# Performance work log

Hardware: AMD Instinct MI355X
Metric: run time of the kernel (lower is better)

The kernel has to match this reference:

```python
import jax, jax.numpy as jnp
import numpy as np

F_MAX = 16  # static max number of frames (torch code uses max(frames) dynamically)
B, C, H, W = 8, 5, 512, 512


def setup_inputs() -> dict:
    key = jax.random.key(0)
    k1, k2 = jax.random.split(key)
    inp = jax.random.normal(k1, (B, C, H, W), dtype=jnp.float32)
    frames = jax.random.randint(k2, (B,), 1, F_MAX + 1)  # n_frames per sample in [1, F_MAX]
    return {"input": inp, "frames": frames}


def _acquire(inp, frames, noise_key):
    b, _, h, w = inp.shape
    ku, kn = jax.random.split(noise_key)
    img = inp[:, :1]                                                   # [B,1,H,W]
    bias = jax.nn.relu(jnp.mean(inp[:, 1:2], axis=(1, 2, 3), keepdims=True))  # [B,1,1,1]
    sampled = img + bias                                               # broadcasts to [B,F_MAX,H,W] below
    center = img + bias                                                # [B,1,H,W]
    # Frechet noise
    fw = jax.nn.relu(inp[:, 2:3])                                      # weight [B,1,H,W]
    fa = jax.nn.relu(inp[:, 3:4])                                      # alpha  [B,1,H,W]
    u = jnp.clip(jax.random.uniform(ku, (b, F_MAX, h, w), dtype=inp.dtype), 1e-6, 1.0 - 1e-6)
    sampled = sampled + fw * (-jnp.log(u)) ** (-fa)                    # [B,F_MAX,H,W]
    center = center + fw * (1.0 / (fa + 1.0)) ** fa
    # Gaussian noise
    gw = jax.nn.relu(inp[:, 4:5])
    sampled = sampled + gw * jax.random.normal(kn, (b, F_MAX, h, w), dtype=inp.dtype)
    acquired_frames = jnp.clip(sampled, 0.0, 1.0)                      # [B,F_MAX,H,W]
    # ragged per-sample mean over first n_frames frames, vectorized via mask
    mask = (jnp.arange(F_MAX)[None, :, None, None] < frames[:, None, None, None]).astype(inp.dtype)
    frames_f = frames.astype(inp.dtype)[:, None, None, None]
    acquired = jnp.sum(acquired_frames * mask, axis=1, keepdims=True) / frames_f  # [B,1,H,W]
    return acquired, jnp.clip(center, 0.0, 1.0)


def reference(input, frames):
    return _acquire(input, frames, jax.random.key(42))
```

## Files before the change

kernel.cpp:

```cpp
#include <hip/hip_runtime.h>
#include <stdint.h>

#define HW 262144
#define ACQ_N 2097152
#define SREG 69632
#define NREG3 208896

#define CNT(b, c) ((((b) << 2) | (c)) << 5)

#define LOG2F(x) __builtin_amdgcn_logf(x)
#define EXP2F(x) __builtin_amdgcn_exp2f(x)
#define SQRTF(x) __builtin_amdgcn_sqrtf(x)
#define RCPF(x)  __builtin_amdgcn_rcpf(x)

#define ROTL(x, r) __builtin_amdgcn_alignbit((x), (x), (32 - (r)) & 31)

static inline void tf2x32_host(uint32_t k0, uint32_t k1, uint32_t c0, uint32_t c1,
                               uint32_t& o0, uint32_t& o1) {
  const uint32_t ks2 = k0 ^ k1 ^ 0x1BD11BDAu;
  uint32_t x0 = c0 + k0, x1 = c1 + k1;
#define TFR(r) { x0 += x1; x1 = (x1 << (r)) | (x1 >> (32 - (r))); x1 ^= x0; }
  TFR(13) TFR(15) TFR(26) TFR(6)
  x0 += k1;  x1 += ks2 + 1u;
  TFR(17) TFR(29) TFR(16) TFR(24)
  x0 += ks2; x1 += k0 + 2u;
  TFR(13) TFR(15) TFR(26) TFR(6)
  x0 += k0;  x1 += k1 + 3u;
  TFR(17) TFR(29) TFR(16) TFR(24)
  x0 += k1;  x1 += ks2 + 4u;
  TFR(13) TFR(15) TFR(26) TFR(6)
  x0 += ks2; x1 += k0 + 5u;
#undef TFR
  o0 = x0; o1 = x1;
}

__device__ __forceinline__ uint32_t rbits32(uint32_t k0, uint32_t k1, uint32_t idx) {
  const uint32_t ks2 = k0 ^ k1 ^ 0x1BD11BDAu;
  uint32_t x0 = k0, x1 = idx + k1;
#define TFR(r) { x0 += x1; x1 = ROTL(x1, r); x1 ^= x0; }
  TFR(13) TFR(15) TFR(26) TFR(6)
  x0 += k1;  x1 += ks2 + 1u;
  TFR(17) TFR(29) TFR(16) TFR(24)
  x0 += ks2; x1 += k0 + 2u;
  TFR(13) TFR(15) TFR(26) TFR(6)
  x0 += k0;  x1 += k1 + 3u;
  TFR(17) TFR(29) TFR(16) TFR(24)
  x0 += k1;  x1 += ks2 + 4u;
  TFR(13) TFR(15) TFR(26) TFR(6)
  x0 += ks2; x1 += k0 + 5u;
#undef TFR
  return x0 ^ x1;
}

__device__ __forceinline__ float unit_from_bits(uint32_t b) {
  return __uint_as_float((b >> 9) | 0x3F800000u) - 1.0f;
}

__device__ __forceinline__ float sqrt2_erfinv(float x) {
  float ome = fmaf(-x, x, 1.0f);
  float w = -0.69314718056f * LOG2F(ome);
  float wn = w - 2.5f;
  float p = 3.974065e-08f;
  p = fmaf(p, wn, 4.854641e-07f);
  p = fmaf(p, wn, -4.982823e-06f);
  p = fmaf(p, wn, -6.210531e-06f);
  p = fmaf(p, wn, 3.091200e-04f);
  p = fmaf(p, wn, -1.773035e-03f);
  p = fmaf(p, wn, -5.908135e-03f);
  p = fmaf(p, wn, 3.488029e-01f);
  p = fmaf(p, wn, 2.123314e+00f);
  if (__builtin_expect(w >= 5.0f, 0)) {
    float wf = SQRTF(w) - 3.0f;
    float q = -2.831458e-04f;
    q = fmaf(q, wf, 1.427657e-04f);
    q = fmaf(q, wf, 1.908260e-03f);
    q = fmaf(q, wf, -5.195013e-03f);
    q = fmaf(q, wf, 8.116892e-03f);
    q = fmaf(q, wf, -1.0779791e-02f);
    q = fmaf(q, wf, 1.3348579e-02f);
    q = fmaf(q, wf, 1.416582e+00f);
    q = fmaf(q, wf, 4.006434e+00f);
    p = q;
  }
  return p * x;
}

__device__ __forceinline__ float loop_fg(float base, float fw, float fa, float gw,
                                         uint32_t idx, int nf,
                                         uint32_t ku0, uint32_t ku1,
                                         uint32_t kn0, uint32_t kn1) {
  float nfa = -fa, fac = fa * 0.52876637294f;
  float acc = 0.0f;
#pragma unroll 2
  for (int f = 0; f < nf; ++f) {
    uint32_t ub = rbits32(ku0, ku1, idx);
    uint32_t nb = rbits32(kn0, kn1, idx);
    idx += (uint32_t)HW;
    float u = fminf(fmaxf(unit_from_bits(ub), 1e-6f), 0.999999f);
    float pw = EXP2F(fmaf(nfa, LOG2F(-LOG2F(u)), fac));
    float z = sqrt2_erfinv(fmaf(unit_from_bits(nb), 2.0f, -0.99999994f));
    float t = fmaf(gw, z, fmaf(fw, pw, base));
    acc += fminf(fmaxf(t, 0.0f), 1.0f);
  }
  return acc * RCPF((float)nf);
}


__global__ __launch_bounds__(256) void bias_partial(const float* __restrict__ inp,
                                                    float* __restrict__ partial,
                                                    uint32_t* __restrict__ counters) {
  if (blockIdx.x == 0) {
    counters[threadIdx.x] = 0u;
    counters[256 + threadIdx.x] = 0u;
    counters[512 + threadIdx.x] = 0u;
    counters[768 + threadIdx.x] = 0u;
  }
  int blk = blockIdx.x;
  int b = blk >> 6, chunk = blk & 63;
  const float4* src = (const float4*)(inp + ((size_t)b * 5 + 1) * HW
                                          + (size_t)chunk * 4096);
  int t = threadIdx.x;
  float s = 0.0f;
#pragma unroll
  for (int k = 0; k < 4; ++k) {
    float4 v = src[t + k * 256];
    s += (v.x + v.y) + (v.z + v.w);
  }
  for (int off = 32; off; off >>= 1) s += __shfl_down(s, off);
  __shared__ float ws4[4];
  if ((t & 63) == 0) ws4[t >> 6] = s;
  __syncthreads();
  if (t == 0) partial[blk] = ws4[0] + ws4[1] + ws4[2] + ws4[3];
}

__global__ __launch_bounds__(256) void scatter_pack(const float* __restrict__ inp,
                                                    const float* __restrict__ partial,
                                                    float* __restrict__ biasv,
                                                    uint32_t* __restrict__ counters,
                                                    uint32_t* __restrict__ remarr,
                                                    float* __restrict__ out) {
  int blk = blockIdx.x;
  int b = blk >> 8, sub = blk & 255;
  int tid = threadIdx.x, lane = tid & 63, wid = tid >> 6;
  const float* pb = inp + (size_t)b * 5 * HW;
  uint64_t below = (1ull << lane) - 1ull;
  int base_i = sub << 10;

  __shared__ float s_bias;
  __shared__ uint32_t swcnt[4][4];
  __shared__ uint32_t sbase[4];

  if (tid < 64) {
    float s = partial[(b << 6) | tid];
    for (int o = 32; o; o >>= 1) s += __shfl_down(s, o);
    if (tid == 0) {
      float bv = fmaxf(s * (1.0f / 262144.0f), 0.0f);
      s_bias = bv;
      if (sub == 0) biasv[b] = bv;
    }
  }

  float img4[4], fw4[4], fa4[4], gw4[4];
  uint32_t cls4[4];
  uint32_t wc1 = 0, wc2 = 0, wc3 = 0;
#pragma unroll
  for (int k = 0; k < 4; ++k) {
    int i = base_i + (k << 8) + tid;
    img4[k]  = pb[i];
    float f2 = pb[2 * HW + i];
    float f3 = pb[3 * HW + i];
    float f4 = pb[4 * HW + i];
    fw4[k] = fmaxf(f2, 0.0f);
    fa4[k] = fmaxf(f3, 0.0f);
    gw4[k] = fmaxf(f4, 0.0f);
    uint32_t cls = (f2 > 0.0f ? 1u : 0u) | (f4 > 0.0f ? 2u : 0u);
    cls4[k] = cls;
    wc1 += (uint32_t)__popcll(__ballot(cls == 1u));
    wc2 += (uint32_t)__popcll(__ballot(cls == 2u));
    wc3 += (uint32_t)__popcll(__ballot(cls == 3u));
  }
  if (lane == 0) {
    swcnt[wid][1] = wc1; swcnt[wid][2] = wc2; swcnt[wid][3] = wc3;
  }
  __syncthreads();
  if (tid < 3) {
    int c = tid + 1;
    uint32_t tot = swcnt[0][c] + swcnt[1][c] + swcnt[2][c] + swcnt[3][c];
    sbase[c] = atomicAdd(&counters[CNT(b, c)], tot);
  }
  __syncthreads();

  uint32_t run1 = sbase[1], run2 = sbase[2], run3 = sbase[3];
#pragma unroll
  for (int w = 0; w < 4; ++w) {
    if (w < wid) { run1 += swcnt[w][1]; run2 += swcnt[w][2]; run3 += swcnt[w][3]; }
  }
  float bias = s_bias;

  uint32_t* rbase = remarr + (size_t)b * NREG3;
  float*    outa  = out + (size_t)b * HW;
  float*    outc  = out + ACQ_N + (size_t)b * HW;

#pragma unroll
  for (int k = 0; k < 4; ++k) {
    int i = base_i + (k << 8) + tid;
    float fw = fw4[k], fa = fa4[k];
    float basev = img4[k] + bias;
    float cpw = EXP2F(-fa * LOG2F(fa + 1.0f));
    float ctr = fminf(fmaxf(fmaf(fw, cpw, basev), 0.0f), 1.0f);
    outc[i] = ctr;

    uint32_t cls = cls4[k];
    if (cls == 0u) outa[i] = ctr;

    uint64_t ba1 = __ballot(cls == 1u);
    uint64_t ba2 = __ballot(cls == 2u);
    uint64_t ba3 = __ballot(cls == 3u);
    if (cls != 0u) {
      uint64_t own  = (cls == 1u) ? ba1 : ((cls == 2u) ? ba2 : ba3);
      uint32_t rbas = (cls == 1u) ? run1 : ((cls == 2u) ? run2 : run3);
      uint32_t roff = (cls - 1u) * (uint32_t)SREG + rbas + (uint32_t)__popcll(own & below);
      rbase[roff] = (uint32_t)i;
    }
    run1 += (uint32_t)__popcll(ba1);
    run2 += (uint32_t)__popcll(ba2);
    run3 += (uint32_t)__popcll(ba3);
  }
}

__global__ __launch_bounds__(256) void acquire_packed(
    const float* __restrict__ inp, const int* __restrict__ frames,
    const float* __restrict__ biasv, const uint32_t* __restrict__ counters,
    const uint32_t* __restrict__ remarr, float* __restrict__ out,
    uint32_t ku0, uint32_t ku1, uint32_t kn0, uint32_t kn1) {
  int c = 3 - (int)blockIdx.z;
  int b = (int)blockIdx.y;
  uint32_t cnt = counters[CNT(b, c)];
  uint32_t bslot = (uint32_t)blockIdx.x << 9;
  if (bslot >= cnt) return;
  int nf = frames[b];
  float rnf = RCPF((float)nf);
  float bias = biasv[b];
  const float* pb = inp + (size_t)b * 5 * HW;
  size_t rb = (size_t)b * NREG3 + (size_t)(c - 1) * SREG;
  uint32_t tid = threadIdx.x;

  uint32_t rem[2]; bool act[2];
#pragma unroll
  for (int k = 0; k < 2; ++k) {
    uint32_t slot = bslot + ((uint32_t)k << 8) + tid;
    act[k] = slot < cnt;
    uint32_t sl = act[k] ? slot : (cnt - 1u);
    rem[k] = remarr[rb + sl];
  }

  uint32_t idx[2]; float acc[2];
#pragma unroll
  for (int k = 0; k < 2; ++k) {
    idx[k] = ((uint32_t)b << 22) + rem[k];
    acc[k] = 0.0f;
  }

  if (c == 3) {
    float base2[2], fw2[2], gw2[2], nfa[2], fac[2];
#pragma unroll
    for (int k = 0; k < 2; ++k) {
      uint32_t r = rem[k];
      base2[k] = pb[r] + bias;
      fw2[k] = fmaxf(pb[2 * HW + r], 0.0f);
      float fa = fmaxf(pb[3 * HW + r], 0.0f);
      gw2[k] = fmaxf(pb[4 * HW + r], 0.0f);
      nfa[k] = -fa; fac[k] = fa * 0.52876637294f;
    }
#pragma unroll 2
    for (int f = 0; f < nf; ++f) {
      uint32_t ub[2], nb[2];
#pragma unroll
      for (int k = 0; k < 2; ++k) ub[k] = rbits32(ku0, ku1, idx[k]);
#pragma unroll
      for (int k = 0; k < 2; ++k) nb[k] = rbits32(kn0, kn1, idx[k]);
#pragma unroll
      for (int k = 0; k < 2; ++k) {
        idx[k] += (uint32_t)HW;
        float u = fminf(fmaxf(unit_from_bits(ub[k]), 1e-6f), 0.999999f);
        float pw = EXP2F(fmaf(nfa[k], LOG2F(-LOG2F(u)), fac[k]));
        float z = sqrt2_erfinv(fmaf(unit_from_bits(nb[k]), 2.0f, -0.99999994f));
        float t = fmaf(gw2[k], z, fmaf(fw2[k], pw, base2[k]));
        acc[k] += fminf(fmaxf(t, 0.0f), 1.0f);
      }
    }
  } else if (c == 1) {
    float base2[2], fw2[2], nfa[2], fac[2];
#pragma unroll
    for (int k = 0; k < 2; ++k) {
      uint32_t r = rem[k];
      base2[k] = pb[r] + bias;
      fw2[k] = fmaxf(pb[2 * HW + r], 0.0f);
      float fa = fmaxf(pb[3 * HW + r], 0.0f);
      nfa[k] = -fa; fac[k] = fa * 0.52876637294f;
    }
#pragma unroll 4
    for (int f = 0; f < nf; ++f) {
      uint32_t ub[2];
#pragma unroll
      for (int k = 0; k < 2; ++k) ub[k] = rbits32(ku0, ku1, idx[k]);
#pragma unroll
      for (int k = 0; k < 2; ++k) {
        idx[k] += (uint32_t)HW;
        float u = fminf(fmaxf(unit_from_bits(ub[k]), 1e-6f), 0.999999f);
        float pw = EXP2F(fmaf(nfa[k], LOG2F(-LOG2F(u)), fac[k]));
        acc[k] += fminf(fmaxf(fmaf(fw2[k], pw, base2[k]), 0.0f), 1.0f);
      }
    }
  } else {
    float base2[2], gw2[2];
#pragma unroll
    for (int k = 0; k < 2; ++k) {
      uint32_t r = rem[k];
      base2[k] = pb[r] + bias;
      gw2[k] = fmaxf(pb[4 * HW + r], 0.0f);
    }
#pragma unroll 4
    for (int f = 0; f < nf; ++f) {
      uint32_t nb[2];
#pragma unroll
      for (int k = 0; k < 2; ++k) nb[k] = rbits32(kn0, kn1, idx[k]);
#pragma unroll
      for (int k = 0; k < 2; ++k) {
        idx[k] += (uint32_t)HW;
        float z = sqrt2_erfinv(fmaf(unit_from_bits(nb[k]), 2.0f, -0.99999994f));
        acc[k] += fminf(fmaxf(fmaf(gw2[k], z, base2[k]), 0.0f), 1.0f);
      }
    }
  }

#pragma unroll
  for (int k = 0; k < 2; ++k)
    if (act[k]) out[(size_t)b * HW + rem[k]] = acc[k] * rnf;
}

__global__ __launch_bounds__(256) void bias_partial_plain(const float* __restrict__ inp,
                                                          float* __restrict__ partial) {
  int blk = blockIdx.x;
  int b = blk >> 6, chunk = blk & 63;
  const float4* src = (const float4*)(inp + ((size_t)b * 5 + 1) * HW
                                          + (size_t)chunk * 4096);
  int t = threadIdx.x;
  float s = 0.0f;
#pragma unroll
  for (int k = 0; k < 4; ++k) {
    float4 v = src[t + k * 256];
    s += (v.x + v.y) + (v.z + v.w);
  }
  for (int off = 32; off; off >>= 1) s += __shfl_down(s, off);
  __shared__ float ws4[4];
  if ((t & 63) == 0) ws4[t >> 6] = s;
  __syncthreads();
  if (t == 0) partial[blk] = ws4[0] + ws4[1] + ws4[2] + ws4[3];
}

__global__ __launch_bounds__(256) void acquire_plain(
    const float* __restrict__ inp, const int* __restrict__ frames,
    const float* __restrict__ partial, float* __restrict__ out,
    uint32_t ku0, uint32_t ku1, uint32_t kn0, uint32_t kn1) {
  int b = blockIdx.x >> 10;
  int rem = ((blockIdx.x & 1023) << 8) | threadIdx.x;
  __shared__ float s_bias;
  if (threadIdx.x < 64) {
    float s = partial[(b << 6) | threadIdx.x];
    for (int off = 32; off; off >>= 1) s += __shfl_down(s, off);
    if (threadIdx.x == 0) s_bias = fmaxf(s * (1.0f / 262144.0f), 0.0f);
  }
  const float* pb = inp + (size_t)b * 5 * HW;
  float img = pb[rem];
  float fw  = fmaxf(pb[2 * HW + rem], 0.0f);
  float fa  = fmaxf(pb[3 * HW + rem], 0.0f);
  float gw  = fmaxf(pb[4 * HW + rem], 0.0f);
  __syncthreads();
  float base = img + s_bias;
  int nf = frames[b];
  uint32_t idx = ((uint32_t)b << 22) + (uint32_t)rem;
  float res = loop_fg(base, fw, fa, gw, idx, nf, ku0, ku1, kn0, kn1);
  out[(size_t)b * HW + rem] = res;
  float cpw = EXP2F(-fa * LOG2F(fa + 1.0f));
  out[ACQ_N + (size_t)b * HW + rem] = fminf(fmaxf(fmaf(fw, cpw, base), 0.0f), 1.0f);
}

extern "C" void kernel_launch(void* const* d_in, const int* in_sizes, int n_in,
                              void* d_out, int out_size, void* d_ws, size_t ws_size,
                              hipStream_t stream) {
  const float* inp    = (const float*)d_in[0];
  const int*   frames = (const int*)d_in[1];
  float* out = (float*)d_out;

  uint32_t ku0, ku1, kn0, kn1;
  tf2x32_host(0u, 42u, 0u, 0u, ku0, ku1);
  tf2x32_host(0u, 42u, 0u, 1u, kn0, kn1);

  float*    partial  = (float*)d_ws;
  float*    biasv    = (float*)((char*)d_ws + 2048);
  uint32_t* counters = (uint32_t*)((char*)d_ws + 4096);
  const size_t need_full = 8192 + (size_t)8 * NREG3 * 4;

  if (ws_size >= need_full) {
    uint32_t* remarr = (uint32_t*)((char*)d_ws + 8192);
    bias_partial<<<dim3(512), dim3(256), 0, stream>>>(inp, partial, counters);
    scatter_pack<<<dim3(2048), dim3(256), 0, stream>>>(inp, partial, biasv,
                                                       counters, remarr, out);
    acquire_packed<<<dim3(136, 8, 3), dim3(256), 0, stream>>>(inp, frames, biasv,
                                                              counters, remarr, out,
                                                              ku0, ku1, kn0, kn1);
  } else {
    bias_partial_plain<<<dim3(512), dim3(256), 0, stream>>>(inp, partial);
    acquire_plain<<<dim3(8192), dim3(256), 0, stream>>>(inp, frames, partial, out,
                                                        ku0, ku1, kn0, kn1);
  }
}
```

Baseline: 142.1 us.

## Merge bias reduction into prep pass and fold center writes into acquire kernel

Removes the separate bias-reduction kernel. Each prep block now writes a per-block partial sum of channel 1 while it classifies pixels and scatters indices. The center output and the class-0 acquired writes move out of the scatter pass into extra blocks of a single acquire kernel, so they can overlap with the heavy per-frame RNG blocks. Each acquire block rebuilds the per-sample bias from 256 partials. Counters are cleared with a memset instead of inside a kernel, which adds redundant per-block reductions and an extra API call.

```diff
diff --git a/kernel.cpp b/kernel.cpp
--- a/kernel.cpp
+++ b/kernel.cpp
@@ -5,6 +5,8 @@
 #define ACQ_N 2097152
 #define SREG 69632
 #define NREG3 208896
+#define NVCLS 3264
+#define NVALL 5312
 
 #define CNT(b, c) ((((b) << 2) | (c)) << 5)
 
@@ -106,39 +108,10 @@
 }
 
 
-__global__ __launch_bounds__(256) void bias_partial(const float* __restrict__ inp,
-                                                    float* __restrict__ partial,
-                                                    uint32_t* __restrict__ counters) {
-  if (blockIdx.x == 0) {
-    counters[threadIdx.x] = 0u;
-    counters[256 + threadIdx.x] = 0u;
-    counters[512 + threadIdx.x] = 0u;
-    counters[768 + threadIdx.x] = 0u;
-  }
-  int blk = blockIdx.x;
-  int b = blk >> 6, chunk = blk & 63;
-  const float4* src = (const float4*)(inp + ((size_t)b * 5 + 1) * HW
-                                          + (size_t)chunk * 4096);
-  int t = threadIdx.x;
-  float s = 0.0f;
-#pragma unroll
-  for (int k = 0; k < 4; ++k) {
-    float4 v = src[t + k * 256];
-    s += (v.x + v.y) + (v.z + v.w);
-  }
-  for (int off = 32; off; off >>= 1) s += __shfl_down(s, off);
-  __shared__ float ws4[4];
-  if ((t & 63) == 0) ws4[t >> 6] = s;
-  __syncthreads();
-  if (t == 0) partial[blk] = ws4[0] + ws4[1] + ws4[2] + ws4[3];
-}
-
-__global__ __launch_bounds__(256) void scatter_pack(const float* __restrict__ inp,
-                                                    const float* __restrict__ partial,
-                                                    float* __restrict__ biasv,
-                                                    uint32_t* __restrict__ counters,
-                                                    uint32_t* __restrict__ remarr,
-                                                    float* __restrict__ out) {
+__global__ __launch_bounds__(256) void prep(const float* __restrict__ inp,
+                                            float* __restrict__ partial,
+                                            uint32_t* __restrict__ counters,
+                                            uint32_t* __restrict__ remarr) {
   int blk = blockIdx.x;
   int b = blk >> 8, sub = blk & 255;
   int tid = threadIdx.x, lane = tid & 63, wid = tid >> 6;
@@ -146,33 +119,25 @@
   uint64_t below = (1ull << lane) - 1ull;
   int base_i = sub << 10;
 
-  __shared__ float s_bias;
+  __shared__ float ws4[4];
   __shared__ uint32_t swcnt[4][4];
   __shared__ uint32_t sbase[4];
 
-  if (tid < 64) {
-    float s = partial[(b << 6) | tid];
+  {
+    const float4* src = (const float4*)(pb + HW + base_i);
+    float4 v = src[tid];
+    float s = (v.x + v.y) + (v.z + v.w);
     for (int o = 32; o; o >>= 1) s += __shfl_down(s, o);
-    if (tid == 0) {
-      float bv = fmaxf(s * (1.0f / 262144.0f), 0.0f);
-      s_bias = bv;
-      if (sub == 0) biasv[b] = bv;
-    }
-  }
-
-  float img4[4], fw4[4], fa4[4], gw4[4];
+    if (lane == 0) ws4[wid] = s;
+  }
+
   uint32_t cls4[4];
   uint32_t wc1 = 0, wc2 = 0, wc3 = 0;
 #pragma unroll
   for (int k = 0; k < 4; ++k) {
     int i = base_i + (k << 8) + tid;
-    img4[k]  = pb[i];
     float f2 = pb[2 * HW + i];
-    float f3 = pb[3 * HW + i];
     float f4 = pb[4 * HW + i];
-    fw4[k] = fmaxf(f2, 0.0f);
-    fa4[k] = fmaxf(f3, 0.0f);
-    gw4[k] = fmaxf(f4, 0.0f);
     uint32_t cls = (f2 > 0.0f ? 1u : 0u) | (f4 > 0.0f ? 2u : 0u);
     cls4[k] = cls;
     wc1 += (uint32_t)__popcll(__ballot(cls == 1u));
@@ -183,6 +148,7 @@
     swcnt[wid][1] = wc1; swcnt[wid][2] = wc2; swcnt[wid][3] = wc3;
   }
   __syncthreads();
+  if (tid == 0) partial[blk] = ws4[0] + ws4[1] + ws4[2] + ws4[3];
   if (tid < 3) {
     int c = tid + 1;
     uint32_t tot = swcnt[0][c] + swcnt[1][c] + swcnt[2][c] + swcnt[3][c];
@@ -195,31 +161,20 @@
   for (int w = 0; w < 4; ++w) {
     if (w < wid) { run1 += swcnt[w][1]; run2 += swcnt[w][2]; run3 += swcnt[w][3]; }
   }
-  float bias = s_bias;
 
   uint32_t* rbase = remarr + (size_t)b * NREG3;
-  float*    outa  = out + (size_t)b * HW;
-  float*    outc  = out + ACQ_N + (size_t)b * HW;
-
 #pragma unroll
   for (int k = 0; k < 4; ++k) {
     int i = base_i + (k << 8) + tid;
-    float fw = fw4[k], fa = fa4[k];
-    float basev = img4[k] + bias;
-    float cpw = EXP2F(-fa * LOG2F(fa + 1.0f));
-    float ctr = fminf(fmaxf(fmaf(fw, cpw, basev), 0.0f), 1.0f);
-    outc[i] = ctr;
-
     uint32_t cls = cls4[k];
-    if (cls == 0u) outa[i] = ctr;
-
     uint64_t ba1 = __ballot(cls == 1u);
     uint64_t ba2 = __ballot(cls == 2u);
     uint64_t ba3 = __ballot(cls == 3u);
     if (cls != 0u) {
       uint64_t own  = (cls == 1u) ? ba1 : ((cls == 2u) ? ba2 : ba3);
       uint32_t rbas = (cls == 1u) ? run1 : ((cls == 2u) ? run2 : run3);
-      uint32_t roff = (cls - 1u) * (uint32_t)SREG + rbas + (uint32_t)__popcll(own & below);
+      uint32_t roff = (cls - 1u) * (uint32_t)SREG + rbas
+                    + (uint32_t)__popcll(own & below);
       rbase[roff] = (uint32_t)i;
     }
     run1 += (uint32_t)__popcll(ba1);
@@ -228,115 +183,166 @@
   }
 }
 
-__global__ __launch_bounds__(256) void acquire_packed(
+__global__ __launch_bounds__(256) void acquire_all(
     const float* __restrict__ inp, const int* __restrict__ frames,
-    const float* __restrict__ biasv, const uint32_t* __restrict__ counters,
+    const float* __restrict__ partial, const uint32_t* __restrict__ counters,
     const uint32_t* __restrict__ remarr, float* __restrict__ out,
     uint32_t ku0, uint32_t ku1, uint32_t kn0, uint32_t kn1) {
-  int c = 3 - (int)blockIdx.z;
-  int b = (int)blockIdx.y;
-  uint32_t cnt = counters[CNT(b, c)];
-  uint32_t bslot = (uint32_t)blockIdx.x << 9;
-  if (bslot >= cnt) return;
-  int nf = frames[b];
-  float rnf = RCPF((float)nf);
-  float bias = biasv[b];
-  const float* pb = inp + (size_t)b * 5 * HW;
-  size_t rb = (size_t)b * NREG3 + (size_t)(c - 1) * SREG;
-  uint32_t tid = threadIdx.x;
-
-  uint32_t rem[2]; bool act[2];
-#pragma unroll
-  for (int k = 0; k < 2; ++k) {
-    uint32_t slot = bslot + ((uint32_t)k << 8) + tid;
-    act[k] = slot < cnt;
-    uint32_t sl = act[k] ? slot : (cnt - 1u);
-    rem[k] = remarr[rb + sl];
-  }
-
-  uint32_t idx[2]; float acc[2];
-#pragma unroll
-  for (int k = 0; k < 2; ++k) {
-    idx[k] = ((uint32_t)b << 22) + rem[k];
-    acc[k] = 0.0f;
-  }
-
-  if (c == 3) {
-    float base2[2], fw2[2], gw2[2], nfa[2], fac[2];
+  int v = (int)blockIdx.x;
+  int tid = threadIdx.x;
+  __shared__ float s_bias;
+
+  if (v < NVCLS) {
+    int ci = v / 1088;
+    int c = 3 - ci;
+    int r = v - ci * 1088;
+    int b = r / 136;
+    int sb = r - b * 136;
+    uint32_t cnt = counters[CNT(b, c)];
+    uint32_t bslot = (uint32_t)sb << 9;
+    if (bslot >= cnt) return;
+
+    if (tid < 64) {
+      int pbase = b << 8;
+      float s = partial[pbase + tid] + partial[pbase + tid + 64]
+              + partial[pbase + tid + 128] + partial[pbase + tid + 192];
+      for (int o = 32; o; o >>= 1) s += __shfl_down(s, o);
+      if (tid == 0) s_bias = fmaxf(s * (1.0f / 262144.0f), 0.0f);
+    }
+
+    int nf = frames[b];
+    float rnf = RCPF((float)nf);
+    const float* pb = inp + (size_t)b * 5 * HW;
+    size_t rb = (size_t)b * NREG3 + (size_t)(c - 1) * SREG;
+
+    uint32_t rem[2]; bool act[2];
 #pragma unroll
     for (int k = 0; k < 2; ++k) {
-      uint32_t r = rem[k];
-      base2[k] = pb[r] + bias;
-      fw2[k] = fmaxf(pb[2 * HW + r], 0.0f);
-      float fa = fmaxf(pb[3 * HW + r], 0.0f);
-      gw2[k] = fmaxf(pb[4 * HW + r], 0.0f);
-      nfa[k] = -fa; fac[k] = fa * 0.52876637294f;
-    }
+      uint32_t slot = bslot + ((uint32_t)k << 8) + (uint32_t)tid;
+      act[k] = slot < cnt;
+      uint32_t sl = act[k] ? slot : (cnt - 1u);
+      rem[k] = remarr[rb + sl];
+    }
+    __syncthreads();
+    float bias = s_bias;
+
+    uint32_t idx[2]; float acc[2];
+#pragma unroll
+    for (int k = 0; k < 2; ++k) {
+      idx[k] = ((uint32_t)b << 22) + rem[k];
+      acc[k] = 0.0f;
+    }
+
+    if (c == 3) {
+      float base2[2], fw2[2], gw2[2], nfa[2], fac[2];
+#pragma unroll
+      for (int k = 0; k < 2; ++k) {
+        uint32_t rr = rem[k];
+        base2[k] = pb[rr] + bias;
+        fw2[k] = fmaxf(pb[2 * HW + rr], 0.0f);
+        float fa = fmaxf(pb[3 * HW + rr], 0.0f);
+        gw2[k] = fmaxf(pb[4 * HW + rr], 0.0f);
+        nfa[k] = -fa; fac[k] = fa * 0.52876637294f;
+      }
 #pragma unroll 2
-    for (int f = 0; f < nf; ++f) {
-      uint32_t ub[2], nb[2];
-#pragma unroll
-      for (int k = 0; k < 2; ++k) ub[k] = rbits32(ku0, ku1, idx[k]);
-#pragma unroll
-      for (int k = 0; k < 2; ++k) nb[k] = rbits32(kn0, kn1, idx[k]);
+      for (int f = 0; f < nf; ++f) {
+        uint32_t ub[2], nb[2];
+#pragma unroll
+        for (int k = 0; k < 2; ++k) ub[k] = rbits32(ku0, ku1, idx[k]);
+#pragma unroll
+        for (int k = 0; k < 2; ++k) nb[k] = rbits32(kn0, kn1, idx[k]);
+#pragma unroll
+        for (int k = 0; k < 2; ++k) {
+          idx[k] += (uint32_t)HW;
+          float u = fminf(fmaxf(unit_from_bits(ub[k]), 1e-6f), 0.999999f);
+          float pw = EXP2F(fmaf(nfa[k], LOG2F(-LOG2F(u)), fac[k]));
+          float z = sqrt2_erfinv(fmaf(unit_from_bits(nb[k]), 2.0f, -0.99999994f));
+          float t = fmaf(gw2[k], z, fmaf(fw2[k], pw, base2[k]));
+          acc[k] += fminf(fmaxf(t, 0.0f), 1.0f);
+        }
+      }
+    } else if (c == 1) {
+      float base2[2], fw2[2], nfa[2], fac[2];
 #pragma unroll
       for (int k = 0; k < 2; ++k) {
-        idx[k] += (uint32_t)HW;
-        float u = fminf(fmaxf(unit_from_bits(ub[k]), 1e-6f), 0.999999f);
-        float pw = EXP2F(fmaf(nfa[k], LOG2F(-LOG2F(u)), fac[k]));
-        float z = sqrt2_erfinv(fmaf(unit_from_bits(nb[k]), 2.0f, -0.99999994f));
-        float t = fmaf(gw2[k], z, fmaf(fw2[k], pw, base2[k]));
-        acc[k] += fminf(fmaxf(t, 0.0f), 1.0f);
-      }
-    }
-  } else if (c == 1) {
-    float base2[2], fw2[2], nfa[2], fac[2];
-#pragma unroll
-    for (int k = 0; k < 2; ++k) {
-      uint32_t r = rem[k];
-      base2[k] = pb[r] + bias;
-      fw2[k] = fmaxf(pb[2 * HW + r], 0.0f);
-      float fa = fmaxf(pb[3 * HW + r], 0.0f);
-      nfa[k] = -fa; fac[k] = fa * 0.52876637294f;
-    }
+        uint32_t rr = rem[k];
+        base2[k] = pb[rr] + bias;
+        fw2[k] = fmaxf(pb[2 * HW + rr], 0.0f);
+        float fa = fmaxf(pb[3 * HW + rr], 0.0f);
+        nfa[k] = -fa; fac[k] = fa * 0.52876637294f;
+      }
 #pragma unroll 4
-    for (int f = 0; f < nf; ++f) {
-      uint32_t ub[2];
-#pragma unroll
-      for (int k = 0; k < 2; ++k) ub[k] = rbits32(ku0, ku1, idx[k]);
+      for (int f = 0; f < nf; ++f) {
+        uint32_t ub[2];
+#pragma unroll
+        for (int k = 0; k < 2; ++k) ub[k] = rbits32(ku0, ku1, idx[k]);
+#pragma unroll
+        for (int k = 0; k < 2; ++k) {
+          idx[k] += (uint32_t)HW;
+          float u = fminf(fmaxf(unit_from_bits(ub[k]), 1e-6f), 0.999999f);
+          float pw = EXP2F(fmaf(nfa[k], LOG2F(-LOG2F(u)), fac[k]));
+          acc[k] += fminf(fmaxf(fmaf(fw2[k], pw, base2[k]), 0.0f), 1.0f);
+        }
+      }
+    } else {
+      float base2[2], gw2[2];
 #pragma unroll
       for (int k = 0; k < 2; ++k) {
-        idx[k] += (uint32_t)HW;
-        float u = fminf(fmaxf(unit_from_bits(ub[k]), 1e-6f), 0.999999f);
-        float pw = EXP2F(fmaf(nfa[k], LOG2F(-LOG2F(u)), fac[k]));
-        acc[k] += fminf(fmaxf(fmaf(fw2[k], pw, base2[k]), 0.0f), 1.0f);
-      }
-    }
+        uint32_t rr = rem[k];
+        base2[k] = pb[rr] + bias;
+        gw2[k] = fmaxf(pb[4 * HW + rr], 0.0f);
+      }
+#pragma unroll 4
+      for (int f = 0; f < nf; ++f) {
+        uint32_t nb[2];
+#pragma unroll
+        for (int k = 0; k < 2; ++k) nb[k] = rbits32(kn0, kn1, idx[k]);
+#pragma unroll
+        for (int k = 0; k < 2; ++k) {
+          idx[k] += (uint32_t)HW;
+          float z = sqrt2_erfinv(fmaf(unit_from_bits(nb[k]), 2.0f, -0.99999994f));
+          acc[k] += fminf(fmaxf(fmaf(gw2[k], z, base2[k]), 0.0f), 1.0f);
+        }
+      }
+    }
+
+#pragma unroll
+    for (int k = 0; k < 2; ++k)
+      if (act[k]) out[(size_t)b * HW + rem[k]] = acc[k] * rnf;
+
   } else {
-    float base2[2], gw2[2];
-#pragma unroll
-    for (int k = 0; k < 2; ++k) {
-      uint32_t r = rem[k];
-      base2[k] = pb[r] + bias;
-      gw2[k] = fmaxf(pb[4 * HW + r], 0.0f);
-    }
-#pragma unroll 4
-    for (int f = 0; f < nf; ++f) {
-      uint32_t nb[2];
-#pragma unroll
-      for (int k = 0; k < 2; ++k) nb[k] = rbits32(kn0, kn1, idx[k]);
-#pragma unroll
-      for (int k = 0; k < 2; ++k) {
-        idx[k] += (uint32_t)HW;
-        float z = sqrt2_erfinv(fmaf(unit_from_bits(nb[k]), 2.0f, -0.99999994f));
-        acc[k] += fminf(fmaxf(fmaf(gw2[k], z, base2[k]), 0.0f), 1.0f);
-      }
-    }
-  }
-
-#pragma unroll
-  for (int k = 0; k < 2; ++k)
-    if (act[k]) out[(size_t)b * HW + rem[k]] = acc[k] * rnf;
+    int d = v - NVCLS;
+    int b = d >> 8, sub = d & 255;
+    int base_i = sub << 10;
+    const float* pb = inp + (size_t)b * 5 * HW;
+
+    if (tid < 64) {
+      int pbase = b << 8;
+      float s = partial[pbase + tid] + partial[pbase + tid + 64]
+              + partial[pbase + tid + 128] + partial[pbase + tid + 192];
+      for (int o = 32; o; o >>= 1) s += __shfl_down(s, o);
+      if (tid == 0) s_bias = fmaxf(s * (1.0f / 262144.0f), 0.0f);
+    }
+    __syncthreads();
+    float bias = s_bias;
+
+    float* outa = out + (size_t)b * HW;
+    float* outc = out + ACQ_N + (size_t)b * HW;
+#pragma unroll
+    for (int k = 0; k < 4; ++k) {
+      int i = base_i + (k << 8) + tid;
+      float img = pb[i];
+      float f2 = pb[2 * HW + i];
+      float f3 = pb[3 * HW + i];
+      float f4 = pb[4 * HW + i];
+      float fw = fmaxf(f2, 0.0f), fa = fmaxf(f3, 0.0f);
+      float basev = img + bias;
+      float cpw = EXP2F(-fa * LOG2F(fa + 1.0f));
+      float ctr = fminf(fmaxf(fmaf(fw, cpw, basev), 0.0f), 1.0f);
+      outc[i] = ctr;
+      if (f2 <= 0.0f && f4 <= 0.0f) outa[i] = ctr;
+    }
+  }
 }
 
 __global__ __launch_bounds__(256) void bias_partial_plain(const float* __restrict__ inp,
@@ -398,21 +404,20 @@
   tf2x32_host(0u, 42u, 0u, 1u, kn0, kn1);
 
   float*    partial  = (float*)d_ws;
-  float*    biasv    = (float*)((char*)d_ws + 2048);
-  uint32_t* counters = (uint32_t*)((char*)d_ws + 4096);
-  const size_t need_full = 8192 + (size_t)8 * NREG3 * 4;
+  uint32_t* counters = (uint32_t*)((char*)d_ws + 8192);
+  uint32_t* remarr   = (uint32_t*)((char*)d_ws + 16384);
+  const size_t need_full = 16384 + (size_t)8 * NREG3 * 4;
 
   if (ws_size >= need_full) {
-    uint32_t* remarr = (uint32_t*)((char*)d_ws + 8192);
-    bias_partial<<<dim3(512), dim3(256), 0, stream>>>(inp, partial, counters);
-    scatter_pack<<<dim3(2048), dim3(256), 0, stream>>>(inp, partial, biasv,
-                                                       counters, remarr, out);
-    acquire_packed<<<dim3(136, 8, 3), dim3(256), 0, stream>>>(inp, frames, biasv,
-                                                              counters, remarr, out,
-                                                              ku0, ku1, kn0, kn1);
+    hipMemsetAsync(counters, 0, 1056 * sizeof(uint32_t), stream);
+    prep<<<dim3(2048), dim3(256), 0, stream>>>(inp, partial, counters, remarr);
+    acquire_all<<<dim3(NVALL), dim3(256), 0, stream>>>(inp, frames, partial,
+                                                       counters, remarr, out,
+                                                       ku0, ku1, kn0, kn1);
   } else {
-    bias_partial_plain<<<dim3(512), dim3(256), 0, stream>>>(inp, partial);
-    acquire_plain<<<dim3(8192), dim3(256), 0, stream>>>(inp, frames, partial, out,
+    float* partialp = (float*)d_ws;
+    bias_partial_plain<<<dim3(512), dim3(256), 0, stream>>>(inp, partialp);
+    acquire_plain<<<dim3(8192), dim3(256), 0, stream>>>(inp, frames, partialp, out,
                                                         ku0, ku1, kn0, kn1);
   }
 }
```

Result: faster. 138.6 us (-2.4%).
